# Kernel tuning notes

Hardware: AMD Instinct MI355X
Metric: run time of the kernel (lower is better)

## Reference

```python
import jax, jax.numpy as jnp
import numpy as np

W_DIM = 512
C_IN = 512
C_OUT = 512
K = 3
EPS = 1e-6
STYLE_SCALE = 1.0 / np.sqrt(W_DIM)              # EqualizedWeight scale for (out,in)
CONV_SCALE = 1.0 / np.sqrt(C_IN * K * K)        # EqualizedWeight scale for (out,in,k,k)


def setup_inputs() -> dict:
    key = jax.random.key(0)
    ks = jax.random.split(key, 6)
    B, H, W = 16, 64, 64
    return {
        "x": jax.random.normal(ks[0], (B, C_IN, H, W), dtype=jnp.float32),
        "w": jax.random.normal(ks[1], (B, W_DIM), dtype=jnp.float32),
        "style_weight": jax.random.normal(ks[2], (C_IN, W_DIM), dtype=jnp.float32),
        "style_bias": jnp.zeros((C_IN,), dtype=jnp.float32),
        "conv_weight": jax.random.normal(ks[3], (C_OUT, C_IN, K, K), dtype=jnp.float32),
        "noise_weight": jax.random.normal(ks[4], (1, C_OUT, 1, 1), dtype=jnp.float32),
        "bias": jnp.zeros((C_OUT,), dtype=jnp.float32),
        "noise": jax.random.normal(ks[5], (B, 1, H, W), dtype=jnp.float32),
    }


def reference(x, w, style_weight, style_bias, conv_weight, noise_weight, bias, noise):
    B, _, H, Wd = x.shape
    # to_style: equalized linear  [B, C_IN]
    s = w @ (style_weight * STYLE_SCALE).T + style_bias
    # modulate: [B, C_OUT, C_IN, K, K]
    wts = (conv_weight * CONV_SCALE)[None] * s[:, None, :, None, None]
    # demodulate
    sigma = jax.lax.rsqrt(jnp.sum(wts * wts, axis=(2, 3, 4)) + EPS)  # [B, C_OUT]
    wts = wts * sigma[:, :, None, None, None]
    # grouped conv with groups = batch
    x_r = x.reshape(1, B * C_IN, H, Wd)
    w_r = wts.reshape(B * C_OUT, C_IN, K, K)
    y = jax.lax.conv_general_dilated(
        x_r, w_r, window_strides=(1, 1), padding=[(1, 1), (1, 1)],
        dimension_numbers=("NCHW", "OIHW", "NCHW"), feature_group_count=B,
    ).reshape(B, C_OUT, H, Wd)
    # noise injection + bias + leaky relu(0.2)
    y = y + noise_weight * noise + bias[None, :, None, None]
    return jax.nn.leaky_relu(y, negative_slope=0.2)
```

## Files before the change

### kernel.cpp

```cpp
#include <hip/hip_runtime.h>


typedef __attribute__((ext_vector_type(8))) short short8;
typedef __attribute__((ext_vector_type(4))) float f32x4;

#define STYLE_SCALE 0.044194173824159216f
#define CONV_SCALE  0.014731391274719742f
#define CS2         (1.0f/4608.0f)

static __device__ __forceinline__ unsigned short f2bf(float x) {
    union { float f; unsigned int u; } a; a.f = x;
    unsigned int r = a.u + 0x7fffu + ((a.u >> 16) & 1u);
    return (unsigned short)(r >> 16);
}

static __device__ __forceinline__ void gl_lds16(const void* g, void* l) {
    __builtin_amdgcn_global_load_lds(
        (const __attribute__((address_space(1))) unsigned int*)g,
        (__attribute__((address_space(3))) unsigned int*)l, 16, 0, 0);
}

__global__ void k_style(const float* __restrict__ w, const float* __restrict__ sw,
                        const float* __restrict__ sb, float* __restrict__ s) {
    int b = blockIdx.y, j0 = blockIdx.x * 64, t = threadIdx.x;
    __shared__ float wl[512];
    __shared__ float part[256];
    wl[t] = w[b*512 + t]; wl[t+256] = w[b*512 + t + 256];
    __syncthreads();
    int jl = t & 63, seg = t >> 6;
    const float4* row = (const float4*)(sw + (size_t)(j0 + jl)*512) + seg*32;
    const float*  wv  = wl + seg*128;
    float acc = 0.f;
#pragma unroll 4
    for (int k = 0; k < 32; ++k) {
        float4 v = row[k];
        acc += v.x*wv[4*k] + v.y*wv[4*k+1] + v.z*wv[4*k+2] + v.w*wv[4*k+3];
    }
    part[t] = acc;
    __syncthreads();
    if (t < 64)
        s[b*512 + j0 + t] = (part[t] + part[t+64] + part[t+128] + part[t+192])
                            * STYLE_SCALE + sb[j0 + t];
}

__global__ void k_wprep(const float* __restrict__ cw, float* __restrict__ csq,
                        unsigned short* __restrict__ cwt) {
    int o = blockIdx.x, t = threadIdx.x;
    __shared__ float row[4608];
    const float4* src = (const float4*)(cw + (size_t)o*4608);
    for (int i = t; i < 1152; i += 256) ((float4*)row)[i] = src[i];
    __syncthreads();
#pragma unroll
    for (int it = 0; it < 2; ++it) {
        int i = t + it*256;
        float a = 0.f;
#pragma unroll
        for (int k = 0; k < 9; ++k) { float v = row[i*9 + k]; a += v*v; }
        csq[(size_t)o*512 + i] = a * CS2;
    }
    for (int p = t; p < 576; p += 256) {
        int ic = p / 36, rem = p % 36;
        int tap = rem >> 2, g = rem & 3;
        int i0 = ic*32 + g*8;
        union { unsigned short us[8]; uint4 q; } u;
#pragma unroll
        for (int j = 0; j < 8; ++j)
            u.us[j] = f2bf(row[(i0 + j)*9 + tap] * CONV_SCALE);
        *(uint4*)(cwt + ((size_t)p*512 + o)*8) = u.q;
    }
}

__global__ void k_sigma(const float* __restrict__ s, const float* __restrict__ csq,
                        float* __restrict__ sig) {
    int b = blockIdx.y, o0 = blockIdx.x * 64, t = threadIdx.x;
    __shared__ float s2l[512];
    __shared__ float part[256];
    float v0 = s[b*512 + t], v1 = s[b*512 + t + 256];
    s2l[t] = v0*v0; s2l[t+256] = v1*v1;
    __syncthreads();
    int ol = t & 63, seg = t >> 6;
    const float4* row = (const float4*)(csq + (size_t)(o0 + ol)*512) + seg*32;
    const float*  sv  = s2l + seg*128;
    float acc = 0.f;
#pragma unroll 4
    for (int k = 0; k < 32; ++k) {
        float4 c = row[k];
        acc += c.x*sv[4*k] + c.y*sv[4*k+1] + c.z*sv[4*k+2] + c.w*sv[4*k+3];
    }
    part[t] = acc;
    __syncthreads();
    if (t < 64)
        sig[b*512 + o0 + t] = 1.0f / sqrtf(part[t] + part[t+64] + part[t+128]
                                           + part[t+192] + 1e-6f);
}

__global__ void k_xt(const float* __restrict__ x, const float* __restrict__ s,
                     unsigned short* __restrict__ xt) {
    int h = blockIdx.x, b = blockIdx.y, t = threadIdx.x;
    __shared__ float tile[64][65];
    __shared__ float sl[64];
    for (int c0 = 0; c0 < 512; c0 += 64) {
        if (t < 64) sl[t] = s[b*512 + c0 + t];
#pragma unroll
        for (int it = 0; it < 4; ++it) {
            int idx = t + it*256;
            int c = idx >> 4, w4 = (idx & 15) * 4;
            float4 v = *(const float4*)(x + ((size_t)(b*512 + c0 + c)*4096) + h*64 + w4);
            tile[c][w4]   = v.x; tile[c][w4+1] = v.y;
            tile[c][w4+2] = v.z; tile[c][w4+3] = v.w;
        }
        __syncthreads();
#pragma unroll
        for (int it = 0; it < 2; ++it) {
            int idx = t + it*256;
            int wq = idx >> 3, c = (idx & 7) * 8;
            union { unsigned short us[8]; uint4 q; } u;
#pragma unroll
            for (int j = 0; j < 8; ++j)
                u.us[j] = f2bf(tile[c + j][wq] * sl[c + j]);
            *(uint4*)(xt + ((size_t)(b*4096 + h*64 + wq)*512 + c0 + c)) = u.q;
        }
        __syncthreads();
    }
}

__global__ __launch_bounds__(256, 2)
void k_conv(const unsigned short* __restrict__ xt, const unsigned short* __restrict__ cwt,
            const float* __restrict__ sig, const float* __restrict__ nw,
            const float* __restrict__ bias, const float* __restrict__ noise,
            float* __restrict__ out) {
    __shared__ short xs_s[10*66*32];
    __shared__ short wsm_s[9*4*64*8];

    const int tid  = threadIdx.x;
    const int lane = tid & 63;
    const int wave = tid >> 6;
    const int quad = lane >> 4;
    const int l15  = lane & 15;

    const int b     = blockIdx.y;
    const int oblk  = blockIdx.x & 7;
    const int pxblk = blockIdx.x >> 3;
    const int o0 = oblk * 64, h0 = pxblk * 8;

    for (int i = tid; i < 10*66*32/2; i += 256) ((unsigned int*)xs_s)[i] = 0u;
    __syncthreads();

    f32x4 acc[2][4][4];
#pragma unroll
    for (int rr = 0; rr < 2; ++rr)
#pragma unroll
        for (int mt = 0; mt < 4; ++mt)
#pragma unroll
            for (int nt = 0; nt < 4; ++nt) acc[rr][mt][nt] = (f32x4){0.f,0.f,0.f,0.f};

    for (int ic = 0; ic < 16; ++ic) {
        for (int q = wave; q < 76; q += 4) {
            if (q < 36) {
                const unsigned short* src = cwt + ((size_t)(ic*36 + q)*512 + o0 + lane)*8;
                gl_lds16(src, wsm_s + q*512);
            } else {
                int xq = q - 36;
                int r = xq >> 2, p0 = (xq & 3) << 4;
                int gr = h0 - 1 + r;
                if (gr >= 0 && gr < 64) {
                    int p  = p0 + (lane >> 2);
                    int cg = (lane & 3) ^ ((lane >> 2) & 3);
                    const unsigned short* src =
                        xt + ((size_t)(b*4096 + gr*64 + p)*512 + ic*32 + cg*8);
                    gl_lds16(src, xs_s + (r*66 + 1 + p0)*32);
                }
            }
        }
        __syncthreads();

#pragma unroll
        for (int tap = 0; tap < 9; ++tap) {
            const int dy = tap / 3, dx = tap % 3;
            short8 af[4];
            const short8* wp = (const short8*)wsm_s;
            const short8* xp = (const short8*)xs_s;
#pragma unroll
            for (int mt = 0; mt < 4; ++mt)
                af[mt] = wp[(tap*4 + quad)*64 + mt*16 + l15];
#pragma unroll
            for (int rr = 0; rr < 2; ++rr) {
                const int row = wave + rr*4 + dy;
                short8 bfr[4];
#pragma unroll
                for (int nt = 0; nt < 4; ++nt) {
                    int wc   = nt*16 + l15 + dx - 1;
                    int col  = wc + 1;
                    int slot = quad ^ (wc & 3);
                    bfr[nt] = xp[(row*66 + col)*4 + slot];
                }
#pragma unroll
                for (int mt = 0; mt < 4; ++mt)
#pragma unroll
                    for (int nt = 0; nt < 4; ++nt)
                        acc[rr][mt][nt] = __builtin_amdgcn_mfma_f32_16x16x32_bf16(
                            af[mt], bfr[nt], acc[rr][mt][nt], 0, 0, 0);
            }
        }
        __syncthreads();
    }

    float nz[2][4];
#pragma unroll
    for (int rr = 0; rr < 2; ++rr) {
        int h = h0 + wave + rr*4;
#pragma unroll
        for (int nt = 0; nt < 4; ++nt) nz[rr][nt] = noise[b*4096 + h*64 + nt*16 + l15];
    }
#pragma unroll
    for (int mt = 0; mt < 4; ++mt) {
#pragma unroll
        for (int r = 0; r < 4; ++r) {
            int o = o0 + mt*16 + quad*4 + r;
            float sg  = sig[b*512 + o];
            float nwv = nw[o], bv = bias[o];
#pragma unroll
            for (int rr = 0; rr < 2; ++rr) {
                int h = h0 + wave + rr*4;
#pragma unroll
                for (int nt = 0; nt < 4; ++nt) {
                    float v = acc[rr][mt][nt][r] * sg + nwv * nz[rr][nt] + bv;
                    v = (v >= 0.f) ? v : 0.2f * v;
                    out[((size_t)(b*512 + o)*4096) + h*64 + nt*16 + l15] = v;
                }
            }
        }
    }
}

extern "C" void kernel_launch(void* const* d_in, const int* in_sizes, int n_in,
                              void* d_out, int out_size, void* d_ws, size_t ws_size,
                              hipStream_t stream) {
    const float* x     = (const float*)d_in[0];
    const float* w     = (const float*)d_in[1];
    const float* sw    = (const float*)d_in[2];
    const float* sb    = (const float*)d_in[3];
    const float* cw    = (const float*)d_in[4];
    const float* nw    = (const float*)d_in[5];
    const float* bias  = (const float*)d_in[6];
    const float* noise = (const float*)d_in[7];
    float* out = (float*)d_out;

    char* ws = (char*)d_ws;
    unsigned short* xt  = (unsigned short*)(ws + 0);
    unsigned short* cwt = (unsigned short*)(ws + 67108864);
    float* s   = (float*)(ws + 71827456);
    float* sig = (float*)(ws + 71860224);
    float* csq = (float*)(ws + 71892992);

    k_wprep<<<512, 256, 0, stream>>>(cw, csq, cwt);
    k_style<<<dim3(8, 16), 256, 0, stream>>>(w, sw, sb, s);
    k_sigma<<<dim3(8, 16), 256, 0, stream>>>(s, csq, sig);
    k_xt   <<<dim3(64, 16), 256, 0, stream>>>(x, s, xt);
    k_conv <<<dim3(64, 16), 256, 0, stream>>>(xt, cwt, sig, nw, bias, noise, out);
}
```

Measured before the change: 491.8 us.

## Assign adjacent output rows per wave and reuse input row fragments across dy taps

Each wave now computes two adjacent output rows instead of rows spaced four apart. The tap loop is reordered by dx, then dy, so a fetched input row fragment can serve both output rows across consecutive dy taps through a rotating pair of register buffers. This cuts LDS reads of the input tile from 72 to 48 fragment loads per wave per channel chunk, while weight fragment loads stay the same. The cost is somewhat higher register pressure from keeping two B buffers live.

After: 489.1 us. No clear change (-0.5%).

```diff
diff --git a/kernel.cpp b/kernel.cpp
--- a/kernel.cpp
+++ b/kernel.cpp
@@ -153,6 +153,9 @@
         for (int mt = 0; mt < 4; ++mt)
 #pragma unroll
             for (int nt = 0; nt < 4; ++nt) acc[rr][mt][nt] = (f32x4){0.f,0.f,0.f,0.f};
+
+    const short8* wp = (const short8*)wsm_s;
+    const short8* xp = (const short8*)xs_s;
 
     for (int ic = 0; ic < 16; ++ic) {
         for (int q = wave; q < 76; q += 4) {
@@ -175,32 +178,45 @@
         __syncthreads();
 
 #pragma unroll
-        for (int tap = 0; tap < 9; ++tap) {
-            const int dy = tap / 3, dx = tap % 3;
-            short8 af[4];
-            const short8* wp = (const short8*)wsm_s;
-            const short8* xp = (const short8*)xs_s;
-#pragma unroll
-            for (int mt = 0; mt < 4; ++mt)
-                af[mt] = wp[(tap*4 + quad)*64 + mt*16 + l15];
-#pragma unroll
-            for (int rr = 0; rr < 2; ++rr) {
-                const int row = wave + rr*4 + dy;
-                short8 bfr[4];
-#pragma unroll
-                for (int nt = 0; nt < 4; ++nt) {
-                    int wc   = nt*16 + l15 + dx - 1;
-                    int col  = wc + 1;
-                    int slot = quad ^ (wc & 3);
-                    bfr[nt] = xp[(row*66 + col)*4 + slot];
-                }
-#pragma unroll
-                for (int mt = 0; mt < 4; ++mt)
-#pragma unroll
-                    for (int nt = 0; nt < 4; ++nt)
-                        acc[rr][mt][nt] = __builtin_amdgcn_mfma_f32_16x16x32_bf16(
-                            af[mt], bfr[nt], acc[rr][mt][nt], 0, 0, 0);
-            }
+        for (int dx = 0; dx < 3; ++dx) {
+            const int col0 = l15 + dx;
+            const int slot = quad ^ ((l15 + dx - 1) & 3);
+            const short8* xbase = xp + slot;
+            short8 bufA[4], bufB[4];
+
+#define LOADB(buf, d) do {                                                  \
+            int rbase = ((2*wave + (d))*66 + col0) * 4;                     \
+            buf[0] = xbase[rbase];        buf[1] = xbase[rbase + 64];       \
+            buf[2] = xbase[rbase + 128];  buf[3] = xbase[rbase + 192];      \
+        } while (0)
+
+#define TAPSTEP(dy, C0, C1) do {                                            \
+            const int tap = (dy)*3 + dx;                                    \
+            short8 af[4];                                                   \
+            _Pragma("unroll")                                               \
+            for (int mt = 0; mt < 4; ++mt)                                  \
+                af[mt] = wp[(tap*4 + quad)*64 + mt*16 + l15];               \
+            _Pragma("unroll")                                               \
+            for (int mt = 0; mt < 4; ++mt) {                                \
+                _Pragma("unroll")                                           \
+                for (int nt = 0; nt < 4; ++nt) {                            \
+                    acc[0][mt][nt] = __builtin_amdgcn_mfma_f32_16x16x32_bf16( \
+                        af[mt], C0[nt], acc[0][mt][nt], 0, 0, 0);           \
+                    acc[1][mt][nt] = __builtin_amdgcn_mfma_f32_16x16x32_bf16( \
+                        af[mt], C1[nt], acc[1][mt][nt], 0, 0, 0);           \
+                }                                                           \
+            }                                                               \
+        } while (0)
+
+            LOADB(bufA, 0);
+            LOADB(bufB, 1);
+            TAPSTEP(0, bufA, bufB);
+            LOADB(bufA, 2);
+            TAPSTEP(1, bufB, bufA);
+            LOADB(bufB, 3);
+            TAPSTEP(2, bufA, bufB);
+#undef LOADB
+#undef TAPSTEP
         }
         __syncthreads();
     }
@@ -208,7 +224,7 @@
     float nz[2][4];
 #pragma unroll
     for (int rr = 0; rr < 2; ++rr) {
-        int h = h0 + wave + rr*4;
+        int h = h0 + 2*wave + rr;
 #pragma unroll
         for (int nt = 0; nt < 4; ++nt) nz[rr][nt] = noise[b*4096 + h*64 + nt*16 + l15];
     }
@@ -221,7 +237,7 @@
             float nwv = nw[o], bv = bias[o];
 #pragma unroll
             for (int rr = 0; rr < 2; ++rr) {
-                int h = h0 + wave + rr*4;
+                int h = h0 + 2*wave + rr;
 #pragma unroll
                 for (int nt = 0; nt < 4; ++nt) {
                     float v = acc[rr][mt][nt][r] * sg + nwv * nz[rr][nt] + bv;
```
